# Performance work log

Hardware: AMD Instinct MI355X
Metric: run time of the kernel (lower is better)

Reference implementation:

```python
import math
import jax, jax.numpy as jnp
import numpy as np

N_HEADS = 16
HIDDEN = 1024
FACTOR = 256
N_DK = HIDDEN // N_HEADS
B, S = 4, 2048


def _linear_params(key, fan_in, fan_out):
    kw, kb = jax.random.split(key)
    bound = 1.0 / math.sqrt(fan_in)
    W = jax.random.uniform(kw, (fan_in, fan_out), jnp.float32, -bound, bound)
    b = jax.random.uniform(kb, (fan_out,), jnp.float32, -bound, bound)
    return W, b


def setup_inputs() -> dict:
    key = jax.random.key(0)
    ks = jax.random.split(key, 12)
    inp = {
        "query": jax.random.normal(ks[0], (B, S, HIDDEN), jnp.float32),
        "key": jax.random.normal(ks[1], (B, S, HIDDEN), jnp.float32),
        "value": jax.random.normal(ks[2], (B, S, HIDDEN), jnp.float32),
        "mask": jax.random.randint(ks[3], (B, S), 0, 2, jnp.int32),
    }
    names = [("pq", HIDDEN, FACTOR), ("tq", FACTOR, HIDDEN),
             ("pk", HIDDEN, FACTOR), ("tk", FACTOR, HIDDEN),
             ("pv", HIDDEN, FACTOR), ("tv", FACTOR, HIDDEN),
             ("po", HIDDEN, FACTOR), ("to", FACTOR, HIDDEN)]
    for i, (nm, fi, fo) in enumerate(names):
        W, b = _linear_params(ks[4 + i], fi, fo)
        inp[f"W{nm}"], inp[f"b{nm}"] = W, b
    return inp


def _factored(x, Wp, bp, Wt, bt):
    # proj -> leaky_relu(0.2) -> tran
    h = jax.nn.leaky_relu(x @ Wp + bp, negative_slope=0.2)
    return h @ Wt + bt


def reference(query, key, value, mask,
              Wpq, bpq, Wtq, btq, Wpk, bpk, Wtk, btk,
              Wpv, bpv, Wtv, btv, Wpo, bpo, Wto, bto):
    bsize = query.shape[0]

    def split_heads(x):  # [B,S,H*Dk] -> [B,H,S,Dk]
        return x.reshape(bsize, -1, N_HEADS, N_DK).transpose(0, 2, 1, 3)

    q = split_heads(_factored(query, Wpq, bpq, Wtq, btq))
    k = split_heads(_factored(key, Wpk, bpk, Wtk, btk))
    v = split_heads(_factored(value, Wpv, bpv, Wtv, btv))

    scores = jnp.einsum("bhqd,bhkd->bhqk", q, k) / math.sqrt(N_DK)
    m = (mask == 0)[:, None, None, :]  # [B,1,1,S]
    scores = jnp.where(m, jnp.float32(-1e20), scores)
    attn = jax.nn.softmax(scores, axis=-1)
    cv = jnp.einsum("bhqk,bhkd->bhqd", attn, v)
    cv = cv.transpose(0, 2, 1, 3).reshape(bsize, -1, N_HEADS * N_DK)
    # dropout omitted (eval mode / deterministic reference)
    return _factored(cv, Wpo, bpo, Wto, bto)
```

## Files before the change

kernel.cpp:

```cpp
#include <hip/hip_runtime.h>
#include <cstdint>
#include <cstddef>

typedef __bf16 bf16_t;
typedef __bf16 bf16x8 __attribute__((ext_vector_type(8)));
typedef float  f32x4  __attribute__((ext_vector_type(4)));
typedef unsigned int uint32x4 __attribute__((ext_vector_type(4)));
typedef unsigned int uint32x2 __attribute__((ext_vector_type(2)));

#define DEV_INLINE __device__ __forceinline__

constexpr int Bsz = 4, Ssz = 2048, HID = 1024, FAC = 256, NH = 16, DKc = 64;
constexpr int Mrows = Bsz * Ssz;
constexpr float QSCALE = 0.18033688011112042f;

struct Ptr8 { const float* p[8]; };
struct Ptr3 { const float* p[3]; };

DEV_INLINE float fast_exp2(float x) {
#if __has_builtin(__builtin_amdgcn_exp2f)
  return __builtin_amdgcn_exp2f(x);
#else
  return exp2f(x);
#endif
}

DEV_INLINE void async16(const void* g, void* l) {
  __builtin_amdgcn_global_load_lds((const __attribute__((address_space(1))) void*)g,
                                   (__attribute__((address_space(3))) void*)l, 16, 0, 0);
}

#define WBAR(N) do { \
  asm volatile("s_waitcnt vmcnt(" #N ") lgkmcnt(0)" ::: "memory"); \
  __builtin_amdgcn_s_barrier(); \
} while (0)

DEV_INLINE int SW(int r) { return (r & 3) | ((r >> 1) & 4); }

__global__ __launch_bounds__(256) void k_prep(Ptr8 w, Ptr8 bsrc, const int* __restrict__ mask,
                                              bf16_t* wpt, bf16_t* wtt,
                                              float* bp, float* bt, float* mf, bf16_t* mb) {
  const int z = blockIdx.z;
  if (z == 8) {
    const int bid = blockIdx.y * 32 + blockIdx.x;
    if (bid >= 64) return;
    const int i = bid * 256 + threadIdx.x;
    if (i < 4 * FAC) bp[i] = bsrc.p[i >> 8][i & 255];
    if (i < 4 * HID) bt[i] = bsrc.p[4 + (i >> 10)][i & 1023];
    if (i < Bsz * Ssz) {
      const float m = (mask[i] != 0) ? 1.f : 0.f;
      mf[i] = m;
      mb[i] = (bf16_t)m;
    }
    return;
  }
  const int K = (z < 4) ? HID : FAC;
  const int N = (z < 4) ? FAC : HID;
  if ((int)(blockIdx.x * 32) >= N || (int)(blockIdx.y * 32) >= K) return;
  __shared__ float t[32][33];
  const float* src = w.p[z];
  bf16_t* dst = (z < 4) ? (wpt + (size_t)z * FAC * HID) : (wtt + (size_t)(z - 4) * FAC * HID);
  const int tx = threadIdx.x & 31, ty = threadIdx.x >> 5;
  const int kb = blockIdx.y * 32, nb = blockIdx.x * 32;
#pragma unroll
  for (int j = 0; j < 4; ++j)
    t[ty + j * 8][tx] = src[(size_t)(kb + ty + j * 8) * N + nb + tx];
  __syncthreads();
#pragma unroll
  for (int j = 0; j < 4; ++j)
    dst[(size_t)(nb + ty + j * 8) * K + kb + tx] = (bf16_t)t[tx][ty + j * 8];
}

__global__ __launch_bounds__(256, 2) void k_gemmP2(Ptr3 Asrc,
                                                   const bf16_t* __restrict__ Bt_,
                                                   const float* __restrict__ biasAll,
                                                   bf16_t* __restrict__ Call) {
  __shared__ __align__(16) bf16_t As[3][64 * 40];
  __shared__ __align__(16) bf16_t Bs[4][128 * 32];

  const int z = blockIdx.z;
  const bf16_t* Bt = Bt_ + (size_t)z * FAC * HID;
  const float* bias = biasAll + z * FAC;
  bf16_t* C = Call + (size_t)z * Mrows * FAC;

  const int tid = threadIdx.x;
  const int lane = tid & 63, wave = tid >> 6;
  const int quad = lane >> 4, l16 = lane & 15;
  const int m0 = blockIdx.y * 64, n0 = blockIdx.x * 128;

  const int brow = wave * 16 + (lane >> 2), bkc = (lane & 3) * 8;
  const bf16_t* gB0 = Bt + (size_t)(n0 + brow) * HID + bkc;
  const bf16_t* gB1 = gB0 + (size_t)64 * HID;

  const int crow = tid >> 2, chalf = (tid & 3) * 8;
  const float* gAf = Asrc.p[z] + (size_t)(m0 + crow) * HID + chalf;

#define ASYNCB(t, buf)                                \
  do {                                                \
    const int k0_ = (t) * 32;                         \
    async16(gB0 + k0_, Bs[buf] + wave * 512);         \
    async16(gB1 + k0_, Bs[buf] + 2048 + wave * 512);  \
  } while (0)

  {
    f32x4 pa = *(const f32x4*)gAf;
    f32x4 pb = *(const f32x4*)(gAf + 4);
    __builtin_amdgcn_sched_barrier(0);
    ASYNCB(0, 0);
    ASYNCB(1, 1);
    union { bf16_t h[8]; uint32x4 u; } o;
#pragma unroll
    for (int j = 0; j < 4; ++j) { o.h[j] = (bf16_t)pa[j]; o.h[4 + j] = (bf16_t)pb[j]; }
    *(uint32x4*)(As[0] + crow * 40 + chalf) = o.u;
  }

  f32x4 acc[4][2] = {};
  constexpr int nk = 32;

  for (int it = 0; it < nk; ++it) {
    f32x4 xa, xb;
    const int k1 = (it + 1) * 32;
    if (it + 1 < nk) {
      xa = *(const f32x4*)(gAf + k1);
      xb = *(const f32x4*)(gAf + k1 + 4);
    }
    __builtin_amdgcn_sched_barrier(0);
    if (it + 2 < nk) ASYNCB(it + 2, (it + 2) & 3);

    if (it + 2 < nk)      WBAR(6);
    else if (it + 1 < nk) WBAR(4);
    else                  WBAR(0);

    const bf16_t* Ac = As[it % 3];
    const bf16_t* Bc = Bs[it & 3];
    bf16x8 af[4], bfr[2];
#pragma unroll
    for (int i = 0; i < 4; ++i)
      af[i] = *(const bf16x8*)(Ac + (i * 16 + l16) * 40 + quad * 8);
#pragma unroll
    for (int i = 0; i < 2; ++i)
      bfr[i] = *(const bf16x8*)(Bc + (wave * 32 + i * 16 + l16) * 32 + quad * 8);
#pragma unroll
    for (int mi = 0; mi < 4; ++mi)
#pragma unroll
      for (int ni = 0; ni < 2; ++ni)
        acc[mi][ni] = __builtin_amdgcn_mfma_f32_16x16x32_bf16(af[mi], bfr[ni], acc[mi][ni], 0, 0, 0);

    if (it + 1 < nk) {
      union { bf16_t h[8]; uint32x4 u; } o;
#pragma unroll
      for (int j = 0; j < 4; ++j) { o.h[j] = (bf16_t)xa[j]; o.h[4 + j] = (bf16_t)xb[j]; }
      *(uint32x4*)(As[(it + 1) % 3] + crow * 40 + chalf) = o.u;
    }
  }
#undef ASYNCB

#pragma unroll
  for (int mi = 0; mi < 4; ++mi) {
    const int rbase = m0 + mi * 16 + quad * 4;
#pragma unroll
    for (int ni = 0; ni < 2; ++ni) {
      const int col = n0 + wave * 32 + ni * 16 + l16;
      const float bv = bias[col];
#pragma unroll
      for (int r = 0; r < 4; ++r) {
        float y = acc[mi][ni][r] + bv;
        y = (y > 0.f) ? y : 0.2f * y;
        C[(size_t)(rbase + r) * FAC + col] = (bf16_t)y;
      }
    }
  }
}

template <int EPI, typename OUT_T>
__global__ __launch_bounds__(256, 2) void k_gemmQ(const bf16_t* __restrict__ Aall,
                                                  const bf16_t* __restrict__ Btall,
                                                  const float* __restrict__ biasAll,
                                                  OUT_T* __restrict__ Call,
                                                  bf16_t* __restrict__ C2,
                                                  const float* __restrict__ rowmul,
                                                  int N, int K,
                                                  long long Az, long long Bz, long long Cz, int biasz) {
  __shared__ __align__(16) bf16_t As[4][128 * 32];
  __shared__ __align__(16) bf16_t Bs[4][128 * 32];

  const int z = blockIdx.z;
  const bf16_t* Bt = Btall + (size_t)z * Bz;
  const float* bias = biasAll + (size_t)z * biasz;
  OUT_T* C = Call + (size_t)z * Cz;

  const int tid = threadIdx.x;
  const int lane = tid & 63, wave = tid >> 6;
  const int quad = lane >> 4, l16 = lane & 15;
  const int wr = wave >> 1, wc = wave & 1;
  const int m0 = blockIdx.y * 128, n0 = blockIdx.x * 128;

  const int arow = wave * 16 + (lane >> 2), akc = (lane & 3) * 8;
  const bf16_t* gB0 = Bt + (size_t)(n0 + arow) * K + akc;
  const bf16_t* gB1 = gB0 + (size_t)64 * K;
  const bf16_t* A = Aall + (size_t)z * Az;
  const bf16_t* gA0 = A + (size_t)(m0 + arow) * K + akc;
  const bf16_t* gA1 = gA0 + (size_t)64 * K;

#define STAGEQ(t, buf)                               \
  do {                                               \
    const int k0_ = (t) * 32;                        \
    async16(gA0 + k0_, As[buf] + wave * 512);        \
    async16(gA1 + k0_, As[buf] + 2048 + wave * 512); \
    async16(gB0 + k0_, Bs[buf] + wave * 512);        \
    async16(gB1 + k0_, Bs[buf] + 2048 + wave * 512); \
  } while (0)

  const int nk = K / 32;
  STAGEQ(0, 0);
  STAGEQ(1, 1);

  f32x4 acc[4][4] = {};

  for (int it = 0; it < nk; ++it) {
    if (it + 2 < nk) STAGEQ(it + 2, (it + 2) & 3);

    if (it + 2 < nk)      WBAR(8);
    else if (it + 1 < nk) WBAR(4);
    else                  WBAR(0);

    const bf16_t* Ac = As[it & 3];
    const bf16_t* Bc = Bs[it & 3];
    bf16x8 af[4], bfr[4];
#pragma unroll
    for (int i = 0; i < 4; ++i)
      af[i] = *(const bf16x8*)(Ac + (wr * 64 + i * 16 + l16) * 32 + quad * 8);
#pragma unroll
    for (int i = 0; i < 4; ++i)
      bfr[i] = *(const bf16x8*)(Bc + (wc * 64 + i * 16 + l16) * 32 + quad * 8);
#pragma unroll
    for (int mi = 0; mi < 4; ++mi)
#pragma unroll
      for (int ni = 0; ni < 4; ++ni)
        acc[mi][ni] = __builtin_amdgcn_mfma_f32_16x16x32_bf16(af[mi], bfr[ni], acc[mi][ni], 0, 0, 0);
  }
#undef STAGEQ

  if (EPI == 1 && z == 2) {
#pragma unroll
    for (int mi = 0; mi < 4; ++mi) {
      const int rbase = m0 + wr * 64 + mi * 16 + quad * 4;
      const int bb = rbase >> 11, s = rbase & 2047;
      float rmv[4];
#pragma unroll
      for (int r = 0; r < 4; ++r) rmv[r] = rowmul[rbase + r];
#pragma unroll
      for (int ni = 0; ni < 4; ++ni) {
        const int col = n0 + wc * 64 + ni * 16 + l16;
        const float bv = bias[col];
        const int hh = col >> 6, d = col & 63;
        union { bf16_t e[4]; uint32x2 u; } p;
#pragma unroll
        for (int r = 0; r < 4; ++r) p.e[r] = (bf16_t)((acc[mi][ni][r] + bv) * rmv[r]);
        *(uint32x2*)(C2 + (((size_t)((bb * NH + hh) * DKc + d)) << 11) + s) = p.u;
      }
    }
    return;
  }

  const float scale = (EPI == 1 && z == 0) ? QSCALE : 1.f;
#pragma unroll
  for (int mi = 0; mi < 4; ++mi) {
    const int rbase = m0 + wr * 64 + mi * 16 + quad * 4;
#pragma unroll
    for (int ni = 0; ni < 4; ++ni) {
      const int col = n0 + wc * 64 + ni * 16 + l16;
      const float bv = bias[col];
#pragma unroll
      for (int r = 0; r < 4; ++r) {
        float y = (acc[mi][ni][r] + bv) * scale;
        if (EPI == 0) y = (y > 0.f) ? y : 0.2f * y;
        C[(size_t)(rbase + r) * N + col] = (OUT_T)y;
      }
    }
  }
}

__global__ __launch_bounds__(512, 2) void k_attn(const bf16_t* __restrict__ qkv,
                                                 const bf16_t* __restrict__ mb,
                                                 bf16_t* __restrict__ cv) {
  __shared__ __align__(16) bf16_t Ks[4][64 * 64];
  __shared__ __align__(16) bf16_t Vt[4][64 * 64];
  __shared__ __align__(16) bf16_t Ml[Ssz];

  const int qt = blockIdx.x, h = blockIdx.y, b = blockIdx.z;
  const bf16_t* qp = qkv;
  const bf16_t* kp = qkv + (size_t)Mrows * HID;
  const bf16_t* vtp = qkv + 2 * (size_t)Mrows * HID + (size_t)(b * NH + h) * DKc * Ssz;

  const int tid = threadIdx.x;
  const int lane = tid & 63, wave = tid >> 6;
  const int quad = lane >> 4, l16 = lane & 15;

  const int r0 = wave * 8 + (lane >> 3);
  const int c0 = ((lane & 7) ^ SW(r0)) * 8;
  const int ldsOff = wave * 512;
  const bf16_t* kgA = kp + (size_t)(b * Ssz + r0) * HID + h * DKc + c0;
  const bf16_t* vgA = vtp + (size_t)r0 * Ssz + c0;

#define STAGEA(t, buf)                                          \
  do {                                                          \
    async16(kgA + (size_t)(t) * 64 * HID, Ks[buf] + ldsOff);    \
    async16(vgA + (t) * 64, Vt[buf] + ldsOff);                  \
  } while (0)

  *(uint32x2*)(Ml + tid * 4) = *(const uint32x2*)(mb + (size_t)b * Ssz + tid * 4);
  STAGEA(0, 0);
  STAGEA(1, 1);

  bf16x8 aq0[4], aq1[4];
#pragma unroll
  for (int g = 0; g < 4; ++g) {
    const size_t qrow = (size_t)(b * Ssz + qt * 512 + g * 128 + wave * 16 + l16) * HID + h * DKc + quad * 8;
    aq0[g] = *(const bf16x8*)(qp + qrow);
    aq1[g] = *(const bf16x8*)(qp + qrow + 32);
  }

  const int krow = 8 * (l16 >> 2) + (l16 & 3);
  f32x4 acc[4][4] = {};
  f32x4 dacc[4] = {};
  const bf16x8 zfrag = {};

  for (int kt = 0; kt < 32; ++kt) {
    if (kt + 2 < 32) STAGEA(kt + 2, (kt + 2) & 3);

    if (kt + 2 < 32)      WBAR(4);
    else if (kt + 1 < 32) WBAR(2);
    else                  WBAR(0);

    const bf16_t* Kc = Ks[kt & 3];
    const bf16_t* Vc = Vt[kt & 3];

    union U { uint32x4 u; bf16x8 h; } ap0[4], ap1[4];
    constexpr int koff[4] = {0, 4, 32, 36};
#pragma unroll
    for (int ks = 0; ks < 4; ++ks) {
      const int row = krow + koff[ks];
      const int sw = SW(row);
      bf16x8 a0 = *(const bf16x8*)(Kc + row * 64 + (quad ^ sw) * 8);
      bf16x8 a1 = *(const bf16x8*)(Kc + row * 64 + ((quad + 4) ^ sw) * 8);
#pragma unroll
      for (int g = 0; g < 4; ++g) {
        f32x4 c = {};
        c = __builtin_amdgcn_mfma_f32_16x16x32_bf16(a0, aq0[g], c, 0, 0, 0);
        c = __builtin_amdgcn_mfma_f32_16x16x32_bf16(a1, aq1[g], c, 0, 0, 0);
        union { bf16_t h[2]; uint32_t u; } p01, p23;
        p01.h[0] = (bf16_t)fast_exp2(c[0]);
        p01.h[1] = (bf16_t)fast_exp2(c[1]);
        p23.h[0] = (bf16_t)fast_exp2(c[2]);
        p23.h[1] = (bf16_t)fast_exp2(c[3]);
        U& t = (ks < 2) ? ap0[g] : ap1[g];
        t.u[(ks & 1) * 2] = p01.u;
        t.u[(ks & 1) * 2 + 1] = p23.u;
      }
    }

    bf16x8 mr0 = *(const bf16x8*)(Ml + kt * 64 + quad * 8);
    bf16x8 mr1 = *(const bf16x8*)(Ml + kt * 64 + 32 + quad * 8);
    if (l16 != 0) { mr0 = zfrag; mr1 = zfrag; }
#pragma unroll
    for (int g = 0; g < 4; ++g) {
      dacc[g] = __builtin_amdgcn_mfma_f32_16x16x32_bf16(ap0[g].h, mr0, dacc[g], 0, 0, 0);
      dacc[g] = __builtin_amdgcn_mfma_f32_16x16x32_bf16(ap1[g].h, mr1, dacc[g], 0, 0, 0);
    }

#pragma unroll
    for (int d = 0; d < 4; ++d) {
      const int row = d * 16 + l16;
      const int sw = SW(row);
      bf16x8 bv0 = *(const bf16x8*)(Vc + row * 64 + (quad ^ sw) * 8);
      bf16x8 bv1 = *(const bf16x8*)(Vc + row * 64 + ((quad + 4) ^ sw) * 8);
#pragma unroll
      for (int g = 0; g < 4; ++g) {
        acc[g][d] = __builtin_amdgcn_mfma_f32_16x16x32_bf16(ap0[g].h, bv0, acc[g][d], 0, 0, 0);
        acc[g][d] = __builtin_amdgcn_mfma_f32_16x16x32_bf16(ap1[g].h, bv1, acc[g][d], 0, 0, 0);
      }
    }
  }
#undef STAGEA

#pragma unroll
  for (int g = 0; g < 4; ++g) {
    const size_t obase = (size_t)(b * Ssz + qt * 512 + g * 128 + wave * 16 + quad * 4) * HID + h * DKc + l16;
#pragma unroll
    for (int r = 0; r < 4; ++r) {
      const float denom = __shfl(dacc[g][r], lane & 48, 64);
      const float rl = 1.f / denom;
#pragma unroll
      for (int d = 0; d < 4; ++d)
        cv[obase + (size_t)r * HID + d * 16] = (bf16_t)(acc[g][d][r] * rl);
    }
  }
}

extern "C" void kernel_launch(void* const* d_in, const int* in_sizes, int n_in,
                              void* d_out, int out_size, void* d_ws, size_t ws_size,
                              hipStream_t stream) {
  (void)in_sizes; (void)n_in; (void)out_size; (void)ws_size;
  const float* q_in = (const float*)d_in[0];
  const float* k_in = (const float*)d_in[1];
  const float* v_in = (const float*)d_in[2];
  const int* mask = (const int*)d_in[3];

  bf16_t* XB = (bf16_t*)d_ws;
  bf16_t* H3 = XB + (size_t)3 * Mrows * HID;
  bf16_t* CV = H3 + (size_t)3 * Mrows * FAC;
  bf16_t* WPT = CV + (size_t)Mrows * HID;
  bf16_t* WTT = WPT + (size_t)4 * FAC * HID;
  float* BP = (float*)(WTT + (size_t)4 * FAC * HID);
  float* BT = BP + 4 * FAC;
  float* MF = BT + 4 * HID;
  bf16_t* MB = (bf16_t*)(MF + Mrows);
  bf16_t* VTg = XB + 2 * (size_t)Mrows * HID;

  Ptr8 w;
  w.p[0] = (const float*)d_in[4];  w.p[1] = (const float*)d_in[8];
  w.p[2] = (const float*)d_in[12]; w.p[3] = (const float*)d_in[16];
  w.p[4] = (const float*)d_in[6];  w.p[5] = (const float*)d_in[10];
  w.p[6] = (const float*)d_in[14]; w.p[7] = (const float*)d_in[18];
  Ptr8 bs;
  bs.p[0] = (const float*)d_in[5];  bs.p[1] = (const float*)d_in[9];
  bs.p[2] = (const float*)d_in[13]; bs.p[3] = (const float*)d_in[17];
  bs.p[4] = (const float*)d_in[7];  bs.p[5] = (const float*)d_in[11];
  bs.p[6] = (const float*)d_in[15]; bs.p[7] = (const float*)d_in[19];
  hipLaunchKernelGGL(k_prep, dim3(32, 32, 9), dim3(256), 0, stream, w, bs, mask,
                     WPT, WTT, BP, BT, MF, MB);

  Ptr3 xs; xs.p[0] = q_in; xs.p[1] = k_in; xs.p[2] = v_in;

  hipLaunchKernelGGL(k_gemmP2, dim3(2, Mrows / 64, 3), dim3(256), 0, stream,
                     xs, WPT, BP, H3);

  hipLaunchKernelGGL((k_gemmQ<1, bf16_t>), dim3(HID / 128, Mrows / 128, 3), dim3(256), 0, stream,
                     H3, WTT, BT, XB, VTg, MF,
                     HID, FAC, (long long)Mrows * FAC, (long long)FAC * HID, (long long)Mrows * HID, HID);

  hipLaunchKernelGGL(k_attn, dim3(Ssz / 512, NH, Bsz), dim3(512), 0, stream, XB, MB, CV);

  hipLaunchKernelGGL((k_gemmQ<0, bf16_t>), dim3(FAC / 128, Mrows / 128, 1), dim3(256), 0, stream,
                     CV, WPT + (size_t)3 * FAC * HID, BP + 3 * FAC, H3, (bf16_t*)nullptr,
                     (const float*)nullptr, FAC, HID, 0LL, 0LL, 0LL, 0);

  hipLaunchKernelGGL((k_gemmQ<2, float>), dim3(HID / 128, Mrows / 128, 1), dim3(256), 0, stream,
                     H3, WTT + (size_t)3 * FAC * HID, BT + 3 * HID, (float*)d_out, (bf16_t*)nullptr,
                     (const float*)nullptr, HID, FAC, 0LL, 0LL, 0LL, 0);
}
```

Measured before the change: 339.0 us.

## Add small-tile output projection GEMM, deepen GEMM pipeline, prioritize attention MFMAs

Replaces the output projection GEMM (N=256, K=1024) with a dedicated 64x64-tile, 128-thread kernel, giving 512 blocks instead of 128 so the grid fills the GPU better. The generic k_gemmQ moves from a 4-buffer, prefetch-distance-2 pipeline to a 5-buffer, prefetch-distance-3 pipeline, which raises LDS use per block. The attention kernel raises wave priority around its MFMA section, and k_gemmP2 gets launch bounds of 3 blocks per SM. The leaky-relu path for EPI==0 is removed from k_gemmQ because that instantiation is no longer used.

```diff
diff --git a/kernel.cpp b/kernel.cpp
--- a/kernel.cpp
+++ b/kernel.cpp
@@ -71,7 +71,7 @@
     dst[(size_t)(nb + ty + j * 8) * K + kb + tx] = (bf16_t)t[tx][ty + j * 8];
 }
 
-__global__ __launch_bounds__(256, 2) void k_gemmP2(Ptr3 Asrc,
+__global__ __launch_bounds__(256, 3) void k_gemmP2(Ptr3 Asrc,
                                                    const bf16_t* __restrict__ Bt_,
                                                    const float* __restrict__ biasAll,
                                                    bf16_t* __restrict__ Call) {
@@ -181,8 +181,8 @@
                                                   const float* __restrict__ rowmul,
                                                   int N, int K,
                                                   long long Az, long long Bz, long long Cz, int biasz) {
-  __shared__ __align__(16) bf16_t As[4][128 * 32];
-  __shared__ __align__(16) bf16_t Bs[4][128 * 32];
+  __shared__ __align__(16) bf16_t As[5][128 * 32];
+  __shared__ __align__(16) bf16_t Bs[5][128 * 32];
 
   const int z = blockIdx.z;
   const bf16_t* Bt = Btall + (size_t)z * Bz;
@@ -214,18 +214,20 @@
   const int nk = K / 32;
   STAGEQ(0, 0);
   STAGEQ(1, 1);
+  STAGEQ(2, 2);
 
   f32x4 acc[4][4] = {};
 
   for (int it = 0; it < nk; ++it) {
-    if (it + 2 < nk) STAGEQ(it + 2, (it + 2) & 3);
-
-    if (it + 2 < nk)      WBAR(8);
+    if (it + 3 < nk) STAGEQ(it + 3, (it + 3) % 5);
+
+    if (it + 3 < nk)      WBAR(12);
+    else if (it + 2 < nk) WBAR(8);
     else if (it + 1 < nk) WBAR(4);
     else                  WBAR(0);
 
-    const bf16_t* Ac = As[it & 3];
-    const bf16_t* Bc = Bs[it & 3];
+    const bf16_t* Ac = As[it % 5];
+    const bf16_t* Bc = Bs[it % 5];
     bf16x8 af[4], bfr[4];
 #pragma unroll
     for (int i = 0; i < 4; ++i)
@@ -274,8 +276,83 @@
 #pragma unroll
       for (int r = 0; r < 4; ++r) {
         float y = (acc[mi][ni][r] + bv) * scale;
-        if (EPI == 0) y = (y > 0.f) ? y : 0.2f * y;
         C[(size_t)(rbase + r) * N + col] = (OUT_T)y;
+      }
+    }
+  }
+}
+
+__global__ __launch_bounds__(128, 2) void k_gemmO(const bf16_t* __restrict__ A,
+                                                  const bf16_t* __restrict__ Bt,
+                                                  const float* __restrict__ bias,
+                                                  bf16_t* __restrict__ C) {
+  __shared__ __align__(16) bf16_t As[5][64 * 32];
+  __shared__ __align__(16) bf16_t Bs[5][64 * 32];
+
+  const int tid = threadIdx.x;
+  const int lane = tid & 63, wave = tid >> 6;
+  const int quad = lane >> 4, l16 = lane & 15;
+  const int m0 = blockIdx.y * 64, n0 = blockIdx.x * 64;
+
+  const int srow = wave * 32 + (lane >> 2), skc = (lane & 3) * 8;
+  const bf16_t* gA0 = A + (size_t)(m0 + srow) * HID + skc;
+  const bf16_t* gA1 = gA0 + (size_t)16 * HID;
+  const bf16_t* gB0 = Bt + (size_t)(n0 + srow) * HID + skc;
+  const bf16_t* gB1 = gB0 + (size_t)16 * HID;
+
+#define STAGEO(t, buf)                                 \
+  do {                                                 \
+    const int k0_ = (t) * 32;                          \
+    async16(gA0 + k0_, As[buf] + wave * 1024);         \
+    async16(gA1 + k0_, As[buf] + wave * 1024 + 512);   \
+    async16(gB0 + k0_, Bs[buf] + wave * 1024);         \
+    async16(gB1 + k0_, Bs[buf] + wave * 1024 + 512);   \
+  } while (0)
+
+  constexpr int nk = HID / 32;
+  STAGEO(0, 0);
+  STAGEO(1, 1);
+  STAGEO(2, 2);
+
+  f32x4 acc[4][2] = {};
+
+  for (int it = 0; it < nk; ++it) {
+    if (it + 3 < nk) STAGEO(it + 3, (it + 3) % 5);
+
+    if (it + 3 < nk)      WBAR(12);
+    else if (it + 2 < nk) WBAR(8);
+    else if (it + 1 < nk) WBAR(4);
+    else                  WBAR(0);
+
+    const bf16_t* Ac = As[it % 5];
+    const bf16_t* Bc = Bs[it % 5];
+    bf16x8 af[4], bfr[2];
+#pragma unroll
+    for (int i = 0; i < 4; ++i)
+      af[i] = *(const bf16x8*)(Ac + (i * 16 + l16) * 32 + quad * 8);
+#pragma unroll
+    for (int i = 0; i < 2; ++i)
+      bfr[i] = *(const bf16x8*)(Bc + (wave * 32 + i * 16 + l16) * 32 + quad * 8);
+#pragma unroll
+    for (int mi = 0; mi < 4; ++mi)
+#pragma unroll
+      for (int ni = 0; ni < 2; ++ni)
+        acc[mi][ni] = __builtin_amdgcn_mfma_f32_16x16x32_bf16(af[mi], bfr[ni], acc[mi][ni], 0, 0, 0);
+  }
+#undef STAGEO
+
+#pragma unroll
+  for (int mi = 0; mi < 4; ++mi) {
+    const int rbase = m0 + mi * 16 + quad * 4;
+#pragma unroll
+    for (int ni = 0; ni < 2; ++ni) {
+      const int col = n0 + wave * 32 + ni * 16 + l16;
+      const float bv = bias[col];
+#pragma unroll
+      for (int r = 0; r < 4; ++r) {
+        float y = acc[mi][ni][r] + bv;
+        y = (y > 0.f) ? y : 0.2f * y;
+        C[(size_t)(rbase + r) * FAC + col] = (bf16_t)y;
       }
     }
   }
@@ -363,6 +440,8 @@
     bf16x8 mr0 = *(const bf16x8*)(Ml + kt * 64 + quad * 8);
     bf16x8 mr1 = *(const bf16x8*)(Ml + kt * 64 + 32 + quad * 8);
     if (l16 != 0) { mr0 = zfrag; mr1 = zfrag; }
+
+    __builtin_amdgcn_s_setprio(1);
 #pragma unroll
     for (int g = 0; g < 4; ++g) {
       dacc[g] = __builtin_amdgcn_mfma_f32_16x16x32_bf16(ap0[g].h, mr0, dacc[g], 0, 0, 0);
@@ -381,6 +460,7 @@
         acc[g][d] = __builtin_amdgcn_mfma_f32_16x16x32_bf16(ap1[g].h, bv1, acc[g][d], 0, 0, 0);
       }
     }
+    __builtin_amdgcn_s_setprio(0);
   }
 #undef STAGEA
 
@@ -442,9 +522,8 @@
 
   hipLaunchKernelGGL(k_attn, dim3(Ssz / 512, NH, Bsz), dim3(512), 0, stream, XB, MB, CV);
 
-  hipLaunchKernelGGL((k_gemmQ<0, bf16_t>), dim3(FAC / 128, Mrows / 128, 1), dim3(256), 0, stream,
-                     CV, WPT + (size_t)3 * FAC * HID, BP + 3 * FAC, H3, (bf16_t*)nullptr,
-                     (const float*)nullptr, FAC, HID, 0LL, 0LL, 0LL, 0);
+  hipLaunchKernelGGL(k_gemmO, dim3(FAC / 64, Mrows / 64, 1), dim3(128), 0, stream,
+                     CV, WPT + (size_t)3 * FAC * HID, BP + 3 * FAC, H3);
 
   hipLaunchKernelGGL((k_gemmQ<2, float>), dim3(HID / 128, Mrows / 128, 1), dim3(256), 0, stream,
                      H3, WTT + (size_t)3 * FAC * HID, BT + 3 * HID, (float*)d_out, (bf16_t*)nullptr,
```

New measurement: 339.9 us. About the same (+0.2%).
